# Kernel optimization log

Measured on AMD Instinct MI355X. Metric: run time of the kernel, lower is better.

## Reference

```python
import jax, jax.numpy as jnp
import numpy as np

KAPPA = 0.5  # decorrelation loss mixing coefficient (init kwarg)


def setup_inputs() -> dict:
    key = jax.random.key(0)
    kx, kw, kb, kd, ki = jax.random.split(key, 5)
    b, l, d = 4, 8192, 1024
    n_samples = int(0.25 * l)  # sample_frac = 0.25
    x = jax.random.normal(kx, (b, l, d), dtype=jnp.float32)
    W = jax.random.normal(kw, (d, d), dtype=jnp.float32) * 0.02
    bias = jax.random.normal(kb, (d,), dtype=jnp.float32) * 0.02
    # decorr_layer is initialized at identity in the module; perturb slightly so the
    # decorrelation matmul is non-trivial (it gets updated during training).
    decorr = jnp.eye(d, dtype=jnp.float32) + 0.01 * jax.random.normal(kd, (d, d), dtype=jnp.float32)
    sample_idx = jax.random.randint(ki, (b, n_samples), 0, l)  # stand-in for torch.multinomial
    return {"x": x, "W": W, "bias": bias, "decorr": decorr, "sample_idx": sample_idx}


def reference(x, W, bias, decorr, sample_idx):
    # Output path: y = x @ (W @ decorr)^T + bias
    y = jnp.einsum('bld,od->blo', x, W @ decorr) + bias

    b, l, d = x.shape
    # Gather sampled tokens: [b, n, d]
    selected = jnp.take_along_axis(x, sample_idx[:, :, None], axis=1)
    xs = (selected @ decorr.T).reshape(-1, d)  # [N, d], N = b*n_samples
    N = xs.shape[0]

    # DecorrLoss, algebraically reduced (same math as diag_embed/outer-product form):
    #   C_n = x_n x_n^T - diag(x_n^2)  (zero diagonal, off-diag x_i x_j)
    #   V_n = diag(x_n^2) - I          (diagonal x_i^2 - 1, zero off-diag)
    X2 = xs * xs                     # [N, d]
    m2 = jnp.mean(X2, axis=0)        # [d], mean of x_i^2
    S = X2.T @ X2                    # [d, d]; S_ij = sum_n x_ni^2 x_nj^2
    denom = jnp.float32(N) * d * d
    correlation_loss = (jnp.sum(S) - jnp.trace(S)) / denom       # mean_n mean_ij C_n^2
    whitening_loss = jnp.sum((X2 - 1.0) ** 2) / denom             # mean_n mean_ij V_n^2

    G = (xs.T @ xs) / N              # mean_n x_n x_n^T
    C_mean = G - jnp.diag(m2)
    V_mean = jnp.diag(m2) - jnp.eye(d, dtype=xs.dtype)
    grad = (1.0 - KAPPA) * C_mean + KAPPA * V_mean

    return y, grad, correlation_loss, whitening_loss
```

## Files before the change

kernel.cpp:

```cpp
#include <hip/hip_runtime.h>
#include <cstdint>
#include <cstddef>

typedef __bf16 bf16x8 __attribute__((ext_vector_type(8)));
typedef float  f32x4  __attribute__((ext_vector_type(4)));
typedef unsigned short u16x4 __attribute__((ext_vector_type(4)));

typedef __attribute__((address_space(1))) void* gas1_t;
typedef __attribute__((address_space(3))) void* las3_t;

__device__ __forceinline__ unsigned short f2bf(float f) {
  union { float f; unsigned u; } v; v.f = f;
  unsigned r = v.u + 0x7fffu + ((v.u >> 16) & 1u);
  return (unsigned short)(r >> 16);
}
__device__ __forceinline__ float bf2f(unsigned short h) {
  union { unsigned u; float f; } v; v.u = ((unsigned)h) << 16;
  return v.f;
}

constexpr int Bc = 4, Lc = 8192, Dc = 1024, NSAMP = 2048;
constexpr int ROWS = Bc * Lc;
constexpr int NSEL = Bc * NSAMP;
constexpr long long Y_ELEMS = (long long)ROWS * Dc;
constexpr long long GRAD_OFF = Y_ELEMS;
constexpr long long LOSS_OFF = GRAD_OFF + (long long)Dc*Dc;

constexpr int BM8 = 256, BN8 = 256;

__device__ __forceinline__ void stage_half(const unsigned short* __restrict__ G,
                                           unsigned short* lds_half,
                                           int row0, int K, long long kbase,
                                           int wave, int srow) {
#pragma unroll
  for (int j = 0; j < 2; ++j) {
    const int w = wave * 2 + j;
    const unsigned short* src = G + (size_t)(row0 + w * 16 + srow) * K + kbase;
    __builtin_amdgcn_global_load_lds((gas1_t)(void*)src,
                                     (las3_t)(lds_half + w * 512), 16, 0, 0);
  }
}

__device__ __forceinline__ void ld4(const unsigned short* base, int l8, bf16x8* dst) {
#pragma unroll
  for (int i = 0; i < 4; ++i)
    dst[i] = *(const bf16x8*)(base + i * 512 + l8);
}

#define PH_WAIT() do {                                        \
    __builtin_amdgcn_s_barrier();                             \
    asm volatile("s_waitcnt lgkmcnt(0)" ::: "memory");        \
    __builtin_amdgcn_sched_barrier(0);                        \
  } while (0)

template<int MODE>
__global__ __launch_bounds__(512, 2)
void gemm_bt8(const unsigned short* __restrict__ A,
              const unsigned short* __restrict__ B,
              float* __restrict__ Cf,
              const float* __restrict__ bias,
              int M, int N, int K) {
  __shared__ unsigned short sA[2 * 16384];
  __shared__ unsigned short sB[2 * 16384];
  const int tid  = threadIdx.x;
  const int lane = tid & 63;
  const int wave = tid >> 6;
  const int wm = wave >> 2;
  const int wn = wave & 3;
  const int q = lane >> 4, r16 = lane & 15;
  const int l8 = lane * 8;
  const int srow = lane & 15;
  const long long scol = (lane >> 4) * 8;

  const int gx   = gridDim.x;
  const int nwg  = gx * gridDim.y;
  const int orig = blockIdx.y * gx + blockIdx.x;
  const int swz  = (orig & 7) * (nwg >> 3) + (orig >> 3);
  const int m0 = (swz / gx) * BM8;
  const int n0 = (swz % gx) * BN8;

  const int nt = K >> 6;

  f32x4 acc[8][4] = {};

  {
    stage_half(A, sA + 0 * 16384 + 0 * 8192, m0, K, 0,            wave, srow ? srow : srow);
  }
  stage_half(A, sA + 0,          m0, K, 0 * 64 + 0 * 32 + scol, wave, srow);
  stage_half(A, sA + 8192,       m0, K, 0 * 64 + 1 * 32 + scol, wave, srow);
  stage_half(B, sB + 0,          n0, K, 0 * 64 + 0 * 32 + scol, wave, srow);
  stage_half(B, sB + 8192,       n0, K, 0 * 64 + 1 * 32 + scol, wave, srow);
  if (nt > 1) {
    stage_half(B, sB + 16384 + 0,    n0, K, 1 * 64 + 0 * 32 + scol, wave, srow);
    stage_half(A, sA + 16384 + 0,    m0, K, 1 * 64 + 0 * 32 + scol, wave, srow);
    stage_half(B, sB + 16384 + 8192, n0, K, 1 * 64 + 1 * 32 + scol, wave, srow);
    asm volatile("s_waitcnt vmcnt(6)" ::: "memory");
  } else {
    asm volatile("s_waitcnt vmcnt(0)" ::: "memory");
  }
  __builtin_amdgcn_s_barrier();

  for (int g = 0; g < nt; ++g) {
    const int buf = (g & 1) * 16384;
    const int nbuf = 16384 - buf;
    bf16x8 af[4], bfv[4];

    ld4(sA + buf + (wm * 8 + 0) * 512, l8, af);
    ld4(sB + buf + (wn * 4)     * 512, l8, bfv);
    if (g + 1 < nt)
      stage_half(A, sA + nbuf + 8192, m0, K, (long long)(g + 1) * 64 + 32 + scol, wave, srow);
    PH_WAIT();
    __builtin_amdgcn_s_setprio(1);
#pragma unroll
    for (int i = 0; i < 4; ++i)
#pragma unroll
      for (int ni = 0; ni < 4; ++ni)
        acc[i][ni] = __builtin_amdgcn_mfma_f32_16x16x32_bf16(af[i], bfv[ni], acc[i][ni], 0, 0, 0);
    __builtin_amdgcn_s_setprio(0);
    __builtin_amdgcn_s_barrier();

    ld4(sA + buf + (wm * 8 + 4) * 512, l8, af);
    if (g + 2 < nt)
      stage_half(B, sB + buf, n0, K, (long long)(g + 2) * 64 + scol, wave, srow);
    PH_WAIT();
    __builtin_amdgcn_s_setprio(1);
#pragma unroll
    for (int i = 0; i < 4; ++i)
#pragma unroll
      for (int ni = 0; ni < 4; ++ni)
        acc[4 + i][ni] = __builtin_amdgcn_mfma_f32_16x16x32_bf16(af[i], bfv[ni], acc[4 + i][ni], 0, 0, 0);
    __builtin_amdgcn_s_setprio(0);
    __builtin_amdgcn_s_barrier();

    ld4(sA + buf + 8192 + (wm * 8 + 0) * 512, l8, af);
    ld4(sB + buf + 8192 + (wn * 4)     * 512, l8, bfv);
    if (g + 2 < nt)
      stage_half(A, sA + buf, m0, K, (long long)(g + 2) * 64 + scol, wave, srow);
    PH_WAIT();
    __builtin_amdgcn_s_setprio(1);
#pragma unroll
    for (int i = 0; i < 4; ++i)
#pragma unroll
      for (int ni = 0; ni < 4; ++ni)
        acc[i][ni] = __builtin_amdgcn_mfma_f32_16x16x32_bf16(af[i], bfv[ni], acc[i][ni], 0, 0, 0);
    __builtin_amdgcn_s_setprio(0);
    __builtin_amdgcn_s_barrier();

    ld4(sA + buf + 8192 + (wm * 8 + 4) * 512, l8, af);
    if (g + 2 < nt)
      stage_half(B, sB + buf + 8192, n0, K, (long long)(g + 2) * 64 + 32 + scol, wave, srow);
    PH_WAIT();
    __builtin_amdgcn_s_setprio(1);
#pragma unroll
    for (int i = 0; i < 4; ++i)
#pragma unroll
      for (int ni = 0; ni < 4; ++ni)
        acc[4 + i][ni] = __builtin_amdgcn_mfma_f32_16x16x32_bf16(af[i], bfv[ni], acc[4 + i][ni], 0, 0, 0);
    __builtin_amdgcn_s_setprio(0);

    if (g + 1 < nt) {
      if (g + 2 < nt) asm volatile("s_waitcnt vmcnt(6)" ::: "memory");
      else            asm volatile("s_waitcnt vmcnt(0)" ::: "memory");
    }
    __builtin_amdgcn_s_barrier();
  }

  const int row0 = m0 + wm * 128 + q * 4;
  const int col0 = n0 + wn * 64 + r16;
  float bv[4] = {0.f, 0.f, 0.f, 0.f};
  if (MODE == 0) {
#pragma unroll
    for (int ni = 0; ni < 4; ++ni) bv[ni] = bias[col0 + ni * 16];
  }
#pragma unroll
  for (int mi = 0; mi < 8; ++mi) {
#pragma unroll
    for (int r = 0; r < 4; ++r) {
      const int row = row0 + mi * 16 + r;
      const size_t base = (size_t)row * N + col0;
#pragma unroll
      for (int ni = 0; ni < 4; ++ni) {
        const size_t o = base + (size_t)ni * 16;
        float v = acc[mi][ni][r];
        if (MODE == 0) __builtin_nontemporal_store(v + bv[ni], &Cf[o]);
        else           Cf[o] = v;
      }
    }
  }
}

constexpr int BM = 128, BN = 128, BK = 64;

template<int MODE>
__global__ void gemm_bt(const unsigned short* __restrict__ A,
                        const unsigned short* __restrict__ B,
                        float* __restrict__ Cf,
                        const float* __restrict__ bias,
                        int M, int N, int K, int kchunk) {
  __shared__ unsigned short sA[BM * BK];
  __shared__ unsigned short sB[BN * BK];
  const int tid  = threadIdx.x;
  const int lane = tid & 63;
  const int wave = tid >> 6;
  const int wm = wave >> 1, wn = wave & 1;
  const int q = lane >> 4, r16 = lane & 15;

  const int gx   = gridDim.x;
  const int nwg  = gx * gridDim.y;
  const int orig = blockIdx.y * gx + blockIdx.x;
  const int swz  = (orig & 7) * (nwg >> 3) + (orig >> 3);
  const int m0 = (swz / gx) * BM;
  const int n0 = (swz % gx) * BN;
  const int kb = blockIdx.z * kchunk;

  const int lrow = lane >> 3;
  const int lcol = (lane & 7) * 8;

  f32x4 acc[4][4] = {};

  for (int k0 = kb; k0 < kb + kchunk; k0 += BK) {
#pragma unroll
    for (int j = 0; j < 4; ++j) {
      const int c = wave * 4 + j;
      const int row = c * 8 + lrow;
      const unsigned short* ga = A + (size_t)(m0 + row) * K + k0 + lcol;
      __builtin_amdgcn_global_load_lds((gas1_t)(void*)ga, (las3_t)(sA + c * 512), 16, 0, 0);
      const unsigned short* gb = B + (size_t)(n0 + row) * K + k0 + lcol;
      __builtin_amdgcn_global_load_lds((gas1_t)(void*)gb, (las3_t)(sB + c * 512), 16, 0, 0);
    }
    __syncthreads();
#pragma unroll
    for (int kk = 0; kk < BK; kk += 32) {
      bf16x8 af[4], bfv[4];
#pragma unroll
      for (int mi = 0; mi < 4; ++mi)
        af[mi] = *(const bf16x8*)(sA + (size_t)(wm*64 + mi*16 + r16) * BK + kk + q*8);
#pragma unroll
      for (int ni = 0; ni < 4; ++ni)
        bfv[ni] = *(const bf16x8*)(sB + (size_t)(wn*64 + ni*16 + r16) * BK + kk + q*8);
#pragma unroll
      for (int mi = 0; mi < 4; ++mi)
#pragma unroll
        for (int ni = 0; ni < 4; ++ni)
          acc[mi][ni] = __builtin_amdgcn_mfma_f32_16x16x32_bf16(af[mi], bfv[ni], acc[mi][ni], 0, 0, 0);
    }
    __syncthreads();
  }

  const int row0 = m0 + wm*64 + q*4;
  const int col0 = n0 + wn*64 + r16;
  float bv[4] = {0.f, 0.f, 0.f, 0.f};
  if (MODE == 0) {
#pragma unroll
    for (int ni = 0; ni < 4; ++ni) bv[ni] = bias[col0 + ni*16];
  }
#pragma unroll
  for (int mi = 0; mi < 4; ++mi) {
#pragma unroll
    for (int r = 0; r < 4; ++r) {
      const int row = row0 + mi*16 + r;
      const size_t base = (size_t)row * N + col0;
#pragma unroll
      for (int ni = 0; ni < 4; ++ni) {
        const size_t o = base + (size_t)ni * 16;
        float v = acc[mi][ni][r];
        if (MODE == 0)      __builtin_nontemporal_store(v + bv[ni], &Cf[o]);
        else if (MODE == 2) Cf[o] = v;
        else                atomicAdd(&Cf[o], v);
      }
    }
  }
}

template<int NT>
__global__ void cvt_f32_bf16(const float* __restrict__ in, unsigned short* __restrict__ out, long long n) {
  long long i = ((long long)blockIdx.x * 256 + threadIdx.x) * 4;
  if (i >= n) return;
  f32x4 v;
  if (NT) v = __builtin_nontemporal_load((const f32x4*)(in + i));
  else    v = *(const f32x4*)(in + i);
  u16x4 o;
  o.x = f2bf(v.x); o.y = f2bf(v.y); o.z = f2bf(v.z); o.w = f2bf(v.w);
  *(u16x4*)(out + i) = o;
}

__global__ void gather_rows(const unsigned short* __restrict__ xb, const int* __restrict__ idx,
                            unsigned short* __restrict__ out) {
  const int blk = blockIdx.x;
  const int b = blk >> 11, n = blk & 2047;
  const int row = idx[b * NSAMP + n];
  const unsigned short* src = xb + ((size_t)b * Lc + row) * Dc;
  unsigned short* dst = out + (size_t)blk * Dc;
  const int c = threadIdx.x * 4;
  *(u16x4*)(dst + c) = *(const u16x4*)(src + c);
}

__global__ void diag_resid(const float* __restrict__ dc, float* __restrict__ cvec) {
  const int i = blockIdx.x * 256 + threadIdx.x;
  if (i >= Dc) return;
  const float v = dc[(size_t)i * Dc + i];
  cvec[i] = v - bf2f(f2bf(v));
}

__global__ void transpose_bf16(const float* __restrict__ in, unsigned short* __restrict__ outT,
                               int R, int C) {
  __shared__ float tile[64][65];
  const int r0 = blockIdx.y * 64, c0 = blockIdx.x * 64;
  const int t = threadIdx.x;
  const int c = t & 63, r4 = t >> 6;
#pragma unroll
  for (int j = 0; j < 16; ++j) {
    const int r = j * 4 + r4;
    tile[r][c] = in[(size_t)(r0 + r) * C + c0 + c];
  }
  __syncthreads();
  const int i = t >> 2, p = t & 3;
  unsigned short* dst = outT + (size_t)(c0 + i) * R + r0 + p * 16;
#pragma unroll
  for (int j = 0; j < 16; j += 4) {
    u16x4 v;
    v.x = f2bf(tile[p*16 + j + 0][i]);
    v.y = f2bf(tile[p*16 + j + 1][i]);
    v.z = f2bf(tile[p*16 + j + 2][i]);
    v.w = f2bf(tile[p*16 + j + 3][i]);
    *(u16x4*)(dst + j) = v;
  }
}

__global__ void xs_stats_transpose(const float* __restrict__ xs, const unsigned short* __restrict__ ab,
                                   const float* __restrict__ cvec,
                                   unsigned short* __restrict__ xsT,
                                   float* __restrict__ m2sum, float* __restrict__ s1g,
                                   float* __restrict__ s2g) {
  __shared__ float tile[64][65];
  const int n0 = blockIdx.x * 64;
  const int i0 = blockIdx.y * 64;
  const int t = threadIdx.x;
  const int c = t & 63, r4 = t >> 6;
  const float ccol = cvec[i0 + c];
#pragma unroll
  for (int j = 0; j < 16; ++j) {
    const int r = j * 4 + r4;
    const size_t o = (size_t)(n0 + r) * Dc + i0 + c;
    tile[r][c] = xs[o] + bf2f(ab[o]) * ccol;
  }
  __syncthreads();
  if (t < 64) {
    float s1 = 0.f, s2 = 0.f;
#pragma unroll
    for (int cc = 0; cc < 64; ++cc) { float v = tile[t][cc]; float v2 = v*v; s1 += v2; s2 += v2*v2; }
    atomicAdd(&s1g[n0 + t], s1);
    atomicAdd(&s2g[n0 + t], s2);
  } else if (t < 128) {
    const int col = t - 64;
    float cs = 0.f;
#pragma unroll
    for (int rr = 0; rr < 64; ++rr) { float v = tile[rr][col]; cs += v*v; }
    atomicAdd(&m2sum[i0 + col], cs);
  }
  const int i = t >> 2, p = t & 3;
  unsigned short* dst = xsT + (size_t)(i0 + i) * NSEL + n0 + p * 16;
#pragma unroll
  for (int j = 0; j < 16; j += 4) {
    u16x4 v;
    v.x = f2bf(tile[p*16 + j + 0][i]);
    v.y = f2bf(tile[p*16 + j + 1][i]);
    v.z = f2bf(tile[p*16 + j + 2][i]);
    v.w = f2bf(tile[p*16 + j + 3][i]);
    *(u16x4*)(dst + j) = v;
  }
}

__global__ void grad_write(const float* __restrict__ G, const float* __restrict__ m2sum,
                           float* __restrict__ out) {
  const int i = blockIdx.x * 256 + threadIdx.x;
  const int r = i >> 10, c = i & 1023;
  float g = G[i] * (0.5f / (float)NSEL);
  if (r == c) g = 0.5f * (m2sum[r] * (1.0f / (float)NSEL) - 1.0f);
  __builtin_nontemporal_store(g, &out[i]);
}

__global__ void finalize_losses(const float* __restrict__ s1g, const float* __restrict__ s2g,
                                float* __restrict__ out2) {
  __shared__ double sa[256], sb[256], sc[256];
  double a = 0, b = 0, c = 0;
  for (int n = threadIdx.x; n < NSEL; n += 256) {
    double s1 = s1g[n], s2 = s2g[n];
    a += s1 * s1; b += s2; c += s1;
  }
  const int t = threadIdx.x;
  sa[t] = a; sb[t] = b; sc[t] = c;
  __syncthreads();
  for (int s = 128; s > 0; s >>= 1) {
    if (t < s) { sa[t] += sa[t+s]; sb[t] += sb[t+s]; sc[t] += sc[t+s]; }
    __syncthreads();
  }
  if (t == 0) {
    const double denom = (double)NSEL * (double)Dc * (double)Dc;
    const double cnt   = (double)NSEL * (double)Dc;
    out2[0] = (float)((sa[0] - sb[0]) / denom);
    out2[1] = (float)((sb[0] - 2.0 * sc[0] + cnt) / denom);
  }
}

extern "C" void kernel_launch(void* const* d_in, const int* in_sizes, int n_in,
                              void* d_out, int out_size, void* d_ws, size_t ws_size,
                              hipStream_t stream) {
  const float* x      = (const float*)d_in[0];
  const float* W      = (const float*)d_in[1];
  const float* bias   = (const float*)d_in[2];
  const float* decorr = (const float*)d_in[3];
  const int*   sidx   = (const int*)d_in[4];
  float* out = (float*)d_out;

  char* w = (char*)d_ws;
  constexpr size_t SZ_XB  = (size_t)ROWS * Dc * 2;
  constexpr size_t SZ_AB  = (size_t)NSEL * Dc * 2;
  constexpr size_t SZ_DT  = (size_t)Dc * Dc * 2;
  constexpr size_t SZ_WB  = (size_t)Dc * Dc * 2;
  constexpr size_t SZ_MB  = (size_t)Dc * Dc * 2;
  constexpr size_t SZ_XS  = (size_t)NSEL * Dc * 4;
  constexpr size_t SZ_XST = (size_t)Dc * NSEL * 2;
  constexpr size_t SZ_MF  = (size_t)Dc * Dc * 4;
  constexpr size_t SZ_GB  = (size_t)Dc * Dc * 4;
  constexpr size_t SZ_M2  = (size_t)Dc * 4;
  constexpr size_t SZ_S1  = (size_t)NSEL * 4;
  constexpr size_t SZ_S2  = (size_t)NSEL * 4;
  constexpr size_t SZ_CV  = (size_t)Dc * 4;

  size_t off = 0;
  unsigned short* xb  = (unsigned short*)(w + off); off += SZ_XB;
  unsigned short* ab  = (unsigned short*)(w + off); off += SZ_AB;
  unsigned short* dT  = (unsigned short*)(w + off); off += SZ_DT;
  unsigned short* wb  = (unsigned short*)(w + off); off += SZ_WB;
  unsigned short* mb  = (unsigned short*)(w + off); off += SZ_MB;
  float*          xsf = (float*)(w + off);          off += SZ_XS;
  unsigned short* xsT = (unsigned short*)(w + off); off += SZ_XST;
  float*          cv  = (float*)(w + off);          off += SZ_CV;
  char*           zbase = w + off;
  float*          Mf  = (float*)(w + off);          off += SZ_MF;
  float*          Gb  = (float*)(w + off);          off += SZ_GB;
  float*          m2s = (float*)(w + off);          off += SZ_M2;
  float*          s1g = (float*)(w + off);          off += SZ_S1;
  float*          s2g = (float*)(w + off);          off += SZ_S2;
  const size_t zbytes = SZ_MF + SZ_GB + SZ_M2 + SZ_S1 + SZ_S2;

  (void)hipMemsetAsync(zbase, 0, zbytes, stream);

  cvt_f32_bf16<1><<<(int)(Y_ELEMS / 1024), 256, 0, stream>>>(x, xb, Y_ELEMS);
  cvt_f32_bf16<0><<<Dc*Dc / 1024, 256, 0, stream>>>(W, wb, (long long)Dc*Dc);
  diag_resid<<<4, 256, 0, stream>>>(decorr, cv);
  transpose_bf16<<<dim3(Dc/64, Dc/64), 256, 0, stream>>>(decorr, dT, Dc, Dc);
  gather_rows<<<NSEL, 256, 0, stream>>>(xb, sidx, ab);

  gemm_bt<3><<<dim3(Dc/BN, Dc/BM, 8), 256, 0, stream>>>(wb, dT, Mf, nullptr, Dc, Dc, Dc, Dc/8);
  cvt_f32_bf16<0><<<Dc*Dc / 1024, 256, 0, stream>>>(Mf, mb, (long long)Dc*Dc);

  gemm_bt8<0><<<dim3(Dc/BN8, ROWS/BM8), 512, 0, stream>>>(xb, mb, out, bias, ROWS, Dc, Dc);

  gemm_bt8<2><<<dim3(Dc/BN8, NSEL/BM8), 512, 0, stream>>>(ab, dT, xsf, nullptr, NSEL, Dc, Dc);

  xs_stats_transpose<<<dim3(NSEL/64, Dc/64), 256, 0, stream>>>(xsf, ab, cv, xsT, m2s, s1g, s2g);

  gemm_bt<3><<<dim3(Dc/BN, Dc/BM, 16), 256, 0, stream>>>(xsT, xsT, Gb, nullptr, Dc, Dc, NSEL, NSEL/16);

  grad_write<<<Dc*Dc / 256, 256, 0, stream>>>(Gb, m2s, out + GRAD_OFF);
  finalize_losses<<<1, 256, 0, stream>>>(s1g, s2g, out + LOSS_OFF);
}
```

Measured before the change: 503.9 us.

## Software-pipeline LDS fragment loads with double register buffers in 256x256 GEMM

```diff
diff --git a/kernel.cpp b/kernel.cpp
--- a/kernel.cpp
+++ b/kernel.cpp
@@ -28,17 +28,17 @@
 
 constexpr int BM8 = 256, BN8 = 256;
 
-__device__ __forceinline__ void stage_half(const unsigned short* __restrict__ G,
-                                           unsigned short* lds_half,
-                                           int row0, int K, long long kbase,
-                                           int wave, int srow) {
-#pragma unroll
-  for (int j = 0; j < 2; ++j) {
-    const int w = wave * 2 + j;
-    const unsigned short* src = G + (size_t)(row0 + w * 16 + srow) * K + kbase;
-    __builtin_amdgcn_global_load_lds((gas1_t)(void*)src,
-                                     (las3_t)(lds_half + w * 512), 16, 0, 0);
-  }
+#define WAITL(N) do { asm volatile("s_waitcnt lgkmcnt(" #N ")" ::: "memory"); \
+                      __builtin_amdgcn_sched_barrier(0); } while (0)
+#define WAITV(N) asm volatile("s_waitcnt vmcnt(" #N ")" ::: "memory")
+
+__device__ __forceinline__ void stage_half2(const unsigned short* src_base,
+                                            unsigned short* lds_wbase,
+                                            int K, long long kofs) {
+#pragma unroll
+  for (int j = 0; j < 2; ++j)
+    __builtin_amdgcn_global_load_lds((gas1_t)(void*)(src_base + (size_t)j * 16 * K + kofs),
+                                     (las3_t)(lds_wbase + j * 512), 16, 0, 0);
 }
 
 __device__ __forceinline__ void ld4(const unsigned short* base, int l8, bf16x8* dst) {
@@ -47,11 +47,15 @@
     dst[i] = *(const bf16x8*)(base + i * 512 + l8);
 }
 
-#define PH_WAIT() do {                                        \
-    __builtin_amdgcn_s_barrier();                             \
-    asm volatile("s_waitcnt lgkmcnt(0)" ::: "memory");        \
-    __builtin_amdgcn_sched_barrier(0);                        \
-  } while (0)
+__device__ __forceinline__ void mfma16(const bf16x8* af, const bf16x8* bv, f32x4 (*acc)[4]) {
+  __builtin_amdgcn_s_setprio(1);
+#pragma unroll
+  for (int i = 0; i < 4; ++i)
+#pragma unroll
+    for (int n = 0; n < 4; ++n)
+      acc[i][n] = __builtin_amdgcn_mfma_f32_16x16x32_bf16(af[i], bv[n], acc[i][n], 0, 0, 0);
+  __builtin_amdgcn_s_setprio(0);
+}
 
 template<int MODE>
 __global__ __launch_bounds__(512, 2)
@@ -70,7 +74,7 @@
   const int q = lane >> 4, r16 = lane & 15;
   const int l8 = lane * 8;
   const int srow = lane & 15;
-  const long long scol = (lane >> 4) * 8;
+  const int scol = (lane >> 4) * 8;
 
   const int gx   = gridDim.x;
   const int nwg  = gx * gridDim.y;
@@ -78,91 +82,66 @@
   const int swz  = (orig & 7) * (nwg >> 3) + (orig >> 3);
   const int m0 = (swz / gx) * BM8;
   const int n0 = (swz % gx) * BN8;
-
   const int nt = K >> 6;
 
+  const unsigned short* As = A + (size_t)(m0 + wave * 32 + srow) * K + scol;
+  const unsigned short* Bs = B + (size_t)(n0 + wave * 32 + srow) * K + scol;
+  unsigned short* sAw = sA + wave * 1024;
+  unsigned short* sBw = sB + wave * 1024;
+
   f32x4 acc[8][4] = {};
-
-  {
-    stage_half(A, sA + 0 * 16384 + 0 * 8192, m0, K, 0,            wave, srow ? srow : srow);
-  }
-  stage_half(A, sA + 0,          m0, K, 0 * 64 + 0 * 32 + scol, wave, srow);
-  stage_half(A, sA + 8192,       m0, K, 0 * 64 + 1 * 32 + scol, wave, srow);
-  stage_half(B, sB + 0,          n0, K, 0 * 64 + 0 * 32 + scol, wave, srow);
-  stage_half(B, sB + 8192,       n0, K, 0 * 64 + 1 * 32 + scol, wave, srow);
+  bf16x8 afA[4], afB[4], bvA[4], bvB[4];
+
+  stage_half2(As, sAw + 0,    K, 0);
+  stage_half2(As, sAw + 8192, K, 32);
+  stage_half2(Bs, sBw + 0,    K, 0);
+  stage_half2(Bs, sBw + 8192, K, 32);
   if (nt > 1) {
-    stage_half(B, sB + 16384 + 0,    n0, K, 1 * 64 + 0 * 32 + scol, wave, srow);
-    stage_half(A, sA + 16384 + 0,    m0, K, 1 * 64 + 0 * 32 + scol, wave, srow);
-    stage_half(B, sB + 16384 + 8192, n0, K, 1 * 64 + 1 * 32 + scol, wave, srow);
-    asm volatile("s_waitcnt vmcnt(6)" ::: "memory");
+    stage_half2(Bs, sBw + 16384,        K, 64);
+    stage_half2(As, sAw + 16384,        K, 64);
+    stage_half2(Bs, sBw + 16384 + 8192, K, 96);
+    WAITV(6);
   } else {
-    asm volatile("s_waitcnt vmcnt(0)" ::: "memory");
+    WAITV(0);
   }
   __builtin_amdgcn_s_barrier();
+  ld4(sA + (wm * 8 + 0) * 512, l8, afA);
+  ld4(sB + (wn * 4)     * 512, l8, bvA);
 
   for (int g = 0; g < nt; ++g) {
-    const int buf = (g & 1) * 16384;
+    const int buf  = (g & 1) << 14;
     const int nbuf = 16384 - buf;
-    bf16x8 af[4], bfv[4];
-
-    ld4(sA + buf + (wm * 8 + 0) * 512, l8, af);
-    ld4(sB + buf + (wn * 4)     * 512, l8, bfv);
-    if (g + 1 < nt)
-      stage_half(A, sA + nbuf + 8192, m0, K, (long long)(g + 1) * 64 + 32 + scol, wave, srow);
-    PH_WAIT();
-    __builtin_amdgcn_s_setprio(1);
-#pragma unroll
-    for (int i = 0; i < 4; ++i)
-#pragma unroll
-      for (int ni = 0; ni < 4; ++ni)
-        acc[i][ni] = __builtin_amdgcn_mfma_f32_16x16x32_bf16(af[i], bfv[ni], acc[i][ni], 0, 0, 0);
-    __builtin_amdgcn_s_setprio(0);
+    const long long kof = (long long)g * 64;
+
     __builtin_amdgcn_s_barrier();
-
-    ld4(sA + buf + (wm * 8 + 4) * 512, l8, af);
-    if (g + 2 < nt)
-      stage_half(B, sB + buf, n0, K, (long long)(g + 2) * 64 + scol, wave, srow);
-    PH_WAIT();
-    __builtin_amdgcn_s_setprio(1);
-#pragma unroll
-    for (int i = 0; i < 4; ++i)
-#pragma unroll
-      for (int ni = 0; ni < 4; ++ni)
-        acc[4 + i][ni] = __builtin_amdgcn_mfma_f32_16x16x32_bf16(af[i], bfv[ni], acc[4 + i][ni], 0, 0, 0);
-    __builtin_amdgcn_s_setprio(0);
+    ld4(sA + buf + (wm * 8 + 4) * 512, l8, afB);
+    if (g + 1 < nt) stage_half2(As, sAw + nbuf + 8192, K, kof + 96);
+    WAITL(4);
+    mfma16(afA, bvA, &acc[0]);
+
     __builtin_amdgcn_s_barrier();
-
-    ld4(sA + buf + 8192 + (wm * 8 + 0) * 512, l8, af);
-    ld4(sB + buf + 8192 + (wn * 4)     * 512, l8, bfv);
-    if (g + 2 < nt)
-      stage_half(A, sA + buf, m0, K, (long long)(g + 2) * 64 + scol, wave, srow);
-    PH_WAIT();
-    __builtin_amdgcn_s_setprio(1);
-#pragma unroll
-    for (int i = 0; i < 4; ++i)
-#pragma unroll
-      for (int ni = 0; ni < 4; ++ni)
-        acc[i][ni] = __builtin_amdgcn_mfma_f32_16x16x32_bf16(af[i], bfv[ni], acc[i][ni], 0, 0, 0);
-    __builtin_amdgcn_s_setprio(0);
+    ld4(sA + buf + 8192 + (wm * 8 + 0) * 512, l8, afA);
+    ld4(sB + buf + 8192 + (wn * 4)     * 512, l8, bvB);
+    if (g + 2 < nt) stage_half2(Bs, sBw + buf, K, kof + 128);
+    WAITL(8);
+    mfma16(afB, bvA, &acc[4]);
+
     __builtin_amdgcn_s_barrier();
-
-    ld4(sA + buf + 8192 + (wm * 8 + 4) * 512, l8, af);
-    if (g + 2 < nt)
-      stage_half(B, sB + buf + 8192, n0, K, (long long)(g + 2) * 64 + 32 + scol, wave, srow);
-    PH_WAIT();
-    __builtin_amdgcn_s_setprio(1);
-#pragma unroll
-    for (int i = 0; i < 4; ++i)
-#pragma unroll
-      for (int ni = 0; ni < 4; ++ni)
-        acc[4 + i][ni] = __builtin_amdgcn_mfma_f32_16x16x32_bf16(af[i], bfv[ni], acc[4 + i][ni], 0, 0, 0);
-    __builtin_amdgcn_s_setprio(0);
-
+    ld4(sA + buf + 8192 + (wm * 8 + 4) * 512, l8, afB);
+    if (g + 2 < nt) stage_half2(As, sAw + buf, K, kof + 128);
+    WAITL(4);
+    mfma16(afA, bvB, &acc[0]);
+
+    if (g + 2 < nt)      { WAITV(4); }
+    else if (g + 1 < nt) { WAITV(0); }
+    __builtin_amdgcn_s_barrier();
     if (g + 1 < nt) {
-      if (g + 2 < nt) asm volatile("s_waitcnt vmcnt(6)" ::: "memory");
-      else            asm volatile("s_waitcnt vmcnt(0)" ::: "memory");
+      ld4(sA + nbuf + (wm * 8 + 0) * 512, l8, afA);
+      ld4(sB + nbuf + (wn * 4)     * 512, l8, bvA);
     }
-    __builtin_amdgcn_s_barrier();
+    if (g + 2 < nt) stage_half2(Bs, sBw + buf + 8192, K, kof + 160);
+    if (g + 1 < nt) { WAITL(8); } else { WAITL(0); }
+    mfma16(afB, bvB, &acc[4]);
   }
 
   const int row0 = m0 + wm * 128 + q * 4;
@@ -458,7 +437,7 @@
 
   gemm_bt8<0><<<dim3(Dc/BN8, ROWS/BM8), 512, 0, stream>>>(xb, mb, out, bias, ROWS, Dc, Dc);
 
-  gemm_bt8<2><<<dim3(Dc/BN8, NSEL/BM8), 512, 0, stream>>>(ab, dT, xsf, nullptr, NSEL, Dc, Dc);
+  gemm_bt<2><<<dim3(Dc/BN, NSEL/BM, 1), 256, 0, stream>>>(ab, dT, xsf, nullptr, NSEL, Dc, Dc, Dc);
 
   xs_stats_transpose<<<dim3(NSEL/64, Dc/64), 256, 0, stream>>>(xsf, ab, cv, xsT, m2s, s1g, s2g);
 
```

Result: faster. 486.4 us (-3.5%).
